# Performance work log

Hardware: AMD Instinct MI355X
Metric: run time of the kernel (lower is better)

Reference implementation:

```python
import jax, jax.numpy as jnp
import numpy as np

SEQ, EMBED, H, QLR, KVLR, RD, VD = 4096, 2048, 16, 512, 512, 64, 128
KD = VD + RD  # full key/query head dim (content + rope)


def _make_rotary_pe(seq_len, dim):
    inv_freq = 1.0 / jnp.power(10000.0, jnp.arange(0, dim, 2) / dim)
    t = jnp.arange(seq_len)
    freqs = jnp.outer(t, inv_freq)  # (seq, dim//2)
    return jnp.sin(freqs), jnp.cos(freqs)


def _apply_rope(x, sin, cos):
    # x: (seq, ..., dim); sin/cos: (seq, dim//2)
    d = x.shape[-1] // 2
    x1, x2 = x[..., :d], x[..., d:]
    sin2 = jnp.concatenate([sin, sin], axis=-1)
    cos2 = jnp.concatenate([cos, cos], axis=-1)
    ne = x.ndim - 2
    sin2 = sin2.reshape(sin2.shape[0], *[1] * ne, sin2.shape[1])
    cos2 = cos2.reshape(cos2.shape[0], *[1] * ne, cos2.shape[1])
    rot = jnp.concatenate([-x2, x1], axis=-1)
    return x * cos2 + rot * sin2


def setup_inputs() -> dict:
    key = jax.random.key(0)
    ks = jax.random.split(key, 8)

    def w(k, out_dim, in_dim):
        return jax.random.normal(k, (out_dim, in_dim), dtype=jnp.float32) * (1.0 / np.sqrt(in_dim))

    x = jax.random.normal(ks[0], (SEQ, EMBED), dtype=jnp.float32)
    mask = jnp.tril(jnp.ones((SEQ, SEQ), dtype=bool))  # causal
    return {
        "x": x,
        "mask": mask,
        "w_q_down": w(ks[1], QLR, EMBED),
        "w_q_up": w(ks[2], H * VD, QLR),
        "w_q_rope": w(ks[3], H * RD, QLR),
        "w_kv_down": w(ks[4], KVLR, EMBED),
        "w_kv_up": w(ks[5], H * 2 * VD, KVLR),
        "w_k_rope": w(ks[6], RD, EMBED),
        "w_out": w(ks[7], EMBED, H * VD),
    }


def reference(x, mask, w_q_down, w_q_up, w_q_rope, w_kv_down, w_kv_up, w_k_rope, w_out):
    seq = x.shape[0]
    # query path through low-rank bottleneck
    c_q = x @ w_q_down.T                                   # (S, QLR)
    q_content = (c_q @ w_q_up.T).reshape(seq, H, VD)       # (S, H, VD)
    q_rope = (c_q @ w_q_rope.T).reshape(seq, H, RD)        # (S, H, RD)
    # kv path through shared low-rank bottleneck
    c_kv = x @ w_kv_down.T                                 # (S, KVLR)
    kv = c_kv @ w_kv_up.T                                  # (S, H*2*VD)
    k_content_flat, v_flat = jnp.split(kv, 2, axis=-1)
    k_content = k_content_flat.reshape(seq, H, VD)
    v = v_flat.reshape(seq, H, VD)
    # shared rope key (one per token, broadcast to heads)
    k_rope_shared = (x @ w_k_rope.T)[:, None, :]           # (S, 1, RD)
    sin, cos = _make_rotary_pe(seq, RD)
    q_rope_rot = _apply_rope(q_rope, sin, cos)             # (S, H, RD)
    k_rope_rot = jnp.tile(_apply_rope(k_rope_shared, sin, cos), (1, H, 1))
    q_final = jnp.concatenate([q_content, q_rope_rot], axis=-1)  # (S, H, KD)
    k_final = jnp.concatenate([k_content, k_rope_rot], axis=-1)  # (S, H, KD)
    # values zero-padded to key dim
    v_padded = jnp.concatenate(
        [v, jnp.zeros((seq, H, RD), dtype=v.dtype)], axis=-1)    # (S, H, KD)
    # scaled dot-product attention per head
    scale = 1.0 / jnp.sqrt(jnp.asarray(KD, dtype=x.dtype))
    scores = jnp.einsum("shd,thd->hst", q_final, k_final) * scale  # (H, S, S)
    scores = jnp.where(mask[None, :, :], scores, jnp.asarray(-1e9, dtype=scores.dtype))
    probs = jax.nn.softmax(scores, axis=-1)
    attn = jnp.einsum("hst,thd->shd", probs, v_padded)             # (S, H, KD)
    attn = attn[..., :VD].reshape(seq, H * VD)                     # drop zero-pad dims
    return attn @ w_out.T                                          # (S, EMBED)
```

## Files before the change

### kernel.cpp

```cpp
#include <hip/hip_runtime.h>


#define SEQ   4096
#define EMBED 2048
#define NHEAD 16
#define QLR   512
#define KVLR  512
#define RD    64
#define VD    128
#define KDIM  192

typedef __attribute__((ext_vector_type(8)))  _Float16 half8;
typedef __attribute__((ext_vector_type(4)))  _Float16 half4;
typedef __attribute__((ext_vector_type(4)))  float    f32x4;
typedef __attribute__((ext_vector_type(16))) float    f32x16;
typedef __attribute__((ext_vector_type(2)))  unsigned int uint2v;
typedef __attribute__((ext_vector_type(4)))  unsigned int uint4v;

__device__ __forceinline__ void gload16(void* lds, const void* g) {
    __builtin_amdgcn_global_load_lds(
        (const __attribute__((address_space(1))) void*)g,
        (__attribute__((address_space(3))) void*)lds, 16, 0, 0);
}

__device__ __forceinline__ unsigned int pkh(float a, float b) {
    auto h = __builtin_amdgcn_cvt_pkrtz(a, b);
    return __builtin_bit_cast(unsigned int, h);
}

__global__ __launch_bounds__(256) void cvt_plain(const float* __restrict__ s,
                                                 _Float16* __restrict__ d, int n8) {
    const int i = blockIdx.x * 256 + threadIdx.x;
    if (i >= n8) return;
    const float4 a = reinterpret_cast<const float4*>(s)[i * 2];
    const float4 b = reinterpret_cast<const float4*>(s)[i * 2 + 1];
    half8 r;
    r[0] = (_Float16)a.x; r[1] = (_Float16)a.y; r[2] = (_Float16)a.z; r[3] = (_Float16)a.w;
    r[4] = (_Float16)b.x; r[5] = (_Float16)b.y; r[6] = (_Float16)b.z; r[7] = (_Float16)b.w;
    reinterpret_cast<half8*>(d)[i] = r;
}

__global__ __launch_bounds__(256) void cvt_down(const float* __restrict__ wqd,
                                                const float* __restrict__ wkvd,
                                                const float* __restrict__ wkr,
                                                _Float16* __restrict__ dst) {
    const int i = blockIdx.x * 256 + threadIdx.x;
    if (i >= 1152 * 2048 / 8) return;
    const int e = i * 8, row = e >> 11, col = e & 2047;
    const float* src = row < 512  ? wqd  + (size_t)row * 2048 + col
                     : row < 1024 ? wkvd + (size_t)(row - 512) * 2048 + col
                     : row < 1088 ? wkr  + (size_t)(row - 1024) * 2048 + col
                                  : nullptr;
    half8 r = {};
    if (src) {
        const float4 a = reinterpret_cast<const float4*>(src)[0];
        const float4 b = reinterpret_cast<const float4*>(src)[1];
        r[0] = (_Float16)a.x; r[1] = (_Float16)a.y; r[2] = (_Float16)a.z; r[3] = (_Float16)a.w;
        r[4] = (_Float16)b.x; r[5] = (_Float16)b.y; r[6] = (_Float16)b.z; r[7] = (_Float16)b.w;
    }
    reinterpret_cast<half8*>(dst)[i] = r;
}

__global__ __launch_bounds__(256) void cvt_qup(const float* __restrict__ wqu,
                                               const float* __restrict__ wqr,
                                               _Float16* __restrict__ dst) {
    const int i = blockIdx.x * 256 + threadIdx.x;
    if (i >= 3072 * 512 / 8) return;
    const int e = i * 8, row = e >> 9, col = e & 511;
    const float* src = row < 2048 ? wqu + (size_t)row * 512 + col
                                  : wqr + (size_t)(row - 2048) * 512 + col;
    const float4 a = reinterpret_cast<const float4*>(src)[0];
    const float4 b = reinterpret_cast<const float4*>(src)[1];
    half8 r;
    r[0] = (_Float16)a.x; r[1] = (_Float16)a.y; r[2] = (_Float16)a.z; r[3] = (_Float16)a.w;
    r[4] = (_Float16)b.x; r[5] = (_Float16)b.y; r[6] = (_Float16)b.z; r[7] = (_Float16)b.w;
    reinterpret_cast<half8*>(dst)[i] = r;
}

template <int EPI>
__global__ __launch_bounds__(256) void gemm_f16(const _Float16* __restrict__ A,
                                                const _Float16* __restrict__ B,
                                                _Float16* __restrict__ o0,
                                                _Float16* __restrict__ o1,
                                                _Float16* __restrict__ o2,
                                                float* __restrict__ of,
                                                int M, int N, int K)
{
    __shared__ _Float16 sA[128 * 64];
    __shared__ _Float16 sB[128 * 64];

    const int tid  = threadIdx.x;
    const int wid  = tid >> 6;
    const int lane = tid & 63;
    const int lr   = lane & 15;
    const int lg   = lane >> 4;
    const int row0 = blockIdx.y * 128;
    const int col0 = blockIdx.x * 128;
    const int war  = (wid >> 1) * 64;
    const int wac  = (wid & 1) * 64;

    const int sr = lane >> 3;
    const int sk = (lane & 7) * 8;
    const _Float16* Ab = A + (size_t)(row0 + wid * 8 + sr) * K + sk;
    const _Float16* Bb = B + (size_t)(col0 + wid * 8 + sr) * K + sk;

    f32x4 acc[4][4] = {};

    for (int k0 = 0; k0 < K; k0 += 64) {
#pragma unroll
        for (int i = 0; i < 4; ++i) {
            const int c = i * 4 + wid;
            gload16((char*)sA + c * 1024, Ab + (size_t)i * 32 * K + k0);
            gload16((char*)sB + c * 1024, Bb + (size_t)i * 32 * K + k0);
        }
        __syncthreads();

#pragma unroll
        for (int kk = 0; kk < 64; kk += 32) {
            half8 a[4], b[4];
#pragma unroll
            for (int i = 0; i < 4; ++i)
                a[i] = *reinterpret_cast<const half8*>(&sA[(war + i * 16 + lr) * 64 + kk + lg * 8]);
#pragma unroll
            for (int j = 0; j < 4; ++j)
                b[j] = *reinterpret_cast<const half8*>(&sB[(wac + j * 16 + lr) * 64 + kk + lg * 8]);
            __builtin_amdgcn_s_setprio(1);
#pragma unroll
            for (int i = 0; i < 4; ++i)
#pragma unroll
                for (int j = 0; j < 4; ++j)
                    acc[i][j] = __builtin_amdgcn_mfma_f32_16x16x32_f16(a[i], b[j], acc[i][j], 0, 0, 0);
            __builtin_amdgcn_s_setprio(0);
        }
        __syncthreads();
    }

#pragma unroll
    for (int i = 0; i < 4; ++i)
#pragma unroll
        for (int j = 0; j < 4; ++j) {
            const int grow0 = row0 + war + i * 16 + lg * 4;
            const int gcol  = col0 + wac + j * 16 + lr;
            if constexpr (EPI == 2) {
                if (gcol >= 2048) {
                    half4 pv;
#pragma unroll
                    for (int r = 0; r < 4; ++r) pv[r] = (_Float16)acc[i][j][r];
                    *reinterpret_cast<half4*>(&o1[(size_t)(gcol - 2048) * SEQ + grow0]) = pv;
                    continue;
                }
            }
#pragma unroll
            for (int r = 0; r < 4; ++r) {
                const int grow = grow0 + r;
                const float v = acc[i][j][r];
                if constexpr (EPI == 0) {
                    if (gcol < 512)       o0[(size_t)grow * 512 + gcol] = (_Float16)v;
                    else if (gcol < 1024) o1[(size_t)grow * 512 + gcol - 512] = (_Float16)v;
                    else if (gcol < 1088) o2[(size_t)grow * 64 + gcol - 1024] = (_Float16)v;
                } else if constexpr (EPI == 1) {
                    if (gcol < 2048)
                        o0[(size_t)grow * (NHEAD * KDIM) + (gcol >> 7) * KDIM + (gcol & 127)] = (_Float16)v;
                    else {
                        const int c = gcol - 2048;
                        o0[(size_t)grow * (NHEAD * KDIM) + (c >> 6) * KDIM + VD + (c & 63)] = (_Float16)v;
                    }
                } else if constexpr (EPI == 2) {
                    o0[((size_t)(gcol >> 7) * SEQ + grow) * KDIM + (gcol & 127)] = (_Float16)v;
                } else {
                    of[(size_t)grow * N + gcol] = v;
                }
            }
        }
}

__global__ __launch_bounds__(256) void rope_kernel(_Float16* __restrict__ qf,
                                                   _Float16* __restrict__ kf,
                                                   const _Float16* __restrict__ ktmp)
{
    __shared__ float s_sin[32], s_cos[32];
    const int s   = blockIdx.x;
    const int tid = threadIdx.x;
    if (tid < 32) {
        const double inv = exp(-(double)tid * (log(10000.0) / 32.0));
        const double ang = (double)s * inv;
        s_sin[tid] = (float)sin(ang);
        s_cos[tid] = (float)cos(ang);
    }
    __syncthreads();

    for (int p = tid; p < NHEAD * 32; p += 256) {
        const int h = p >> 5, i = p & 31;
        const size_t base = (size_t)s * (NHEAD * KDIM) + h * KDIM + VD;
        const float x1 = (float)qf[base + i];
        const float x2 = (float)qf[base + 32 + i];
        const float cs = s_cos[i], sn = s_sin[i];
        qf[base + i]      = (_Float16)(x1 * cs - x2 * sn);
        qf[base + 32 + i] = (_Float16)(x2 * cs + x1 * sn);
    }
    if (tid < 32) {
        const int i = tid;
        const float x1 = (float)ktmp[(size_t)s * RD + i];
        const float x2 = (float)ktmp[(size_t)s * RD + 32 + i];
        const float cs = s_cos[i], sn = s_sin[i];
        const _Float16 r1 = (_Float16)(x1 * cs - x2 * sn);
        const _Float16 r2 = (_Float16)(x2 * cs + x1 * sn);
#pragma unroll
        for (int h = 0; h < NHEAD; ++h) {
            const size_t base = ((size_t)h * SEQ + s) * KDIM + VD;
            kf[base + i]      = r1;
            kf[base + 32 + i] = r2;
        }
    }
}

__global__ __launch_bounds__(256, 2) void fattn(const _Float16* __restrict__ qf,
                                                const _Float16* __restrict__ kf,
                                                const _Float16* __restrict__ vT,
                                                _Float16* __restrict__ attn)
{
    __shared__ _Float16 sK[2][64 * 192];
    __shared__ _Float16 sV[128 * 64];

    const int idx = blockIdx.x;
    const int h   = idx & 15;
    const int j   = idx >> 4;
    const int qt  = (j < 16) ? (31 - 2 * j) : (2 * (j - 16));
    const int q0  = qt * 128;

    const int tid  = threadIdx.x;
    const int wid  = tid >> 6;
    const int lane = tid & 63;
    const int l31  = lane & 31;
    const int h5   = lane >> 5;
    const int x7   = l31 & 7;
    const int qg   = q0 + wid * 32 + l31;
    const int q0w  = q0 + wid * 32;

    const float scale = 0.0721687836487032f;

    const _Float16* ksrc[6];
    int klds[6];
#pragma unroll
    for (int i = 0; i < 6; ++i) {
        const int c   = wid * 6 + i;
        const int gi  = c * 64 + lane;
        const int row = gi / 24;
        const int g   = gi % 24;
        ksrc[i] = kf + ((size_t)h * SEQ + row) * KDIM + ((g ^ (row & 7)) << 3);
        klds[i] = c * 1024;
    }
    const _Float16* vsrc[4];
    int vlds[4];
#pragma unroll
    for (int i = 0; i < 4; ++i) {
        const int c = wid * 4 + i;
        const int d = c * 8 + (lane >> 3);
        vsrc[i] = vT + ((size_t)h * VD + d) * SEQ + (((lane & 7) ^ (lane >> 3)) << 3);
        vlds[i] = c * 1024;
    }

    half8 qfr[12];
    {
        const _Float16* qb_ = qf + (size_t)qg * (NHEAD * KDIM) + h * KDIM + h5 * 8;
#pragma unroll
        for (int ks = 0; ks < 12; ++ks)
            qfr[ks] = *reinterpret_cast<const half8*>(qb_ + ks * 16);
    }

    f32x16 o0 = {}, o1 = {}, o2 = {}, o3 = {};
    float m_ = -1e30f, l_ = 0.0f;

    const int nt = 2 * qt + 2;

    {
#pragma unroll
        for (int i = 0; i < 6; ++i) gload16((char*)sK[0] + klds[i], ksrc[i]);
#pragma unroll
        for (int i = 0; i < 4; ++i) gload16((char*)sV + vlds[i], vsrc[i]);
    }
    __syncthreads();

    int cur = 0;
    for (int t = 0; t < nt; ++t) {
        const int j0 = t * 64;

        if (t + 1 < nt) {
            const size_t joff = (size_t)(j0 + 64) * KDIM;
#pragma unroll
            for (int i = 0; i < 6; ++i)
                gload16((char*)sK[cur ^ 1] + klds[i], ksrc[i] + joff);
        }

        f32x16 s0 = {}, s1 = {};
        {
            const char* kb = (const char*)sK[cur];
            __builtin_amdgcn_s_setprio(1);
#pragma unroll
            for (int ks = 0; ks < 12; ++ks) {
                const int go = ((ks * 2 + h5) ^ x7) << 4;
                const half8 ka = *reinterpret_cast<const half8*>(kb + l31 * 384 + go);
                const half8 kc = *reinterpret_cast<const half8*>(kb + (32 + l31) * 384 + go);
                s0 = __builtin_amdgcn_mfma_f32_32x32x16_f16(ka, qfr[ks], s0, 0, 0, 0);
                s1 = __builtin_amdgcn_mfma_f32_32x32x16_f16(kc, qfr[ks], s1, 0, 0, 0);
            }
            __builtin_amdgcn_s_setprio(0);
        }

#pragma unroll
        for (int m = 0; m < 16; ++m) { s0[m] *= scale; s1[m] *= scale; }
        if (j0 + 63 > q0w) {
#pragma unroll
            for (int m = 0; m < 16; ++m) {
                const int kv = j0 + (m & 3) + 8 * (m >> 2) + 4 * h5;
                if (kv > qg)      s0[m] = -3.0e38f;
                if (kv + 32 > qg) s1[m] = -3.0e38f;
            }
        }

        float mx = s0[0];
#pragma unroll
        for (int m = 1; m < 16; ++m) mx = fmaxf(mx, s0[m]);
#pragma unroll
        for (int m = 0; m < 16; ++m) mx = fmaxf(mx, s1[m]);
        mx = fmaxf(mx, __shfl_xor(mx, 32, 64));

        if (!__all(mx - m_ <= 8.0f)) {
            const float mn = fmaxf(m_, mx);
            const float alpha = __expf(m_ - mn);
            m_ = mn;
            l_ *= alpha;
#pragma unroll
            for (int m = 0; m < 16; ++m) {
                o0[m] *= alpha; o1[m] *= alpha; o2[m] *= alpha; o3[m] *= alpha;
            }
        }
        float rs = 0.0f;
#pragma unroll
        for (int m = 0; m < 16; ++m) { const float p = __expf(s0[m] - m_); s0[m] = p; rs += p; }
#pragma unroll
        for (int m = 0; m < 16; ++m) { const float p = __expf(s1[m] - m_); s1[m] = p; rs += p; }
        rs += __shfl_xor(rs, 32, 64);
        l_ += rs;

        half8 pb0, pb1, pb2, pb3;
        {
            unsigned int x, x2, y, y2;
            x  = pkh(s0[0], s0[1]);  x2 = pkh(s0[2], s0[3]);
            y  = pkh(s0[4], s0[5]);  y2 = pkh(s0[6], s0[7]);
            uint2v r1 = __builtin_amdgcn_permlane32_swap(x, y, false, false);
            uint2v r2 = __builtin_amdgcn_permlane32_swap(x2, y2, false, false);
            { uint4v u = { r1[0], r2[0], r1[1], r2[1] }; pb0 = __builtin_bit_cast(half8, u); }
            x  = pkh(s0[8], s0[9]);  x2 = pkh(s0[10], s0[11]);
            y  = pkh(s0[12], s0[13]); y2 = pkh(s0[14], s0[15]);
            r1 = __builtin_amdgcn_permlane32_swap(x, y, false, false);
            r2 = __builtin_amdgcn_permlane32_swap(x2, y2, false, false);
            { uint4v u = { r1[0], r2[0], r1[1], r2[1] }; pb1 = __builtin_bit_cast(half8, u); }
            x  = pkh(s1[0], s1[1]);  x2 = pkh(s1[2], s1[3]);
            y  = pkh(s1[4], s1[5]);  y2 = pkh(s1[6], s1[7]);
            r1 = __builtin_amdgcn_permlane32_swap(x, y, false, false);
            r2 = __builtin_amdgcn_permlane32_swap(x2, y2, false, false);
            { uint4v u = { r1[0], r2[0], r1[1], r2[1] }; pb2 = __builtin_bit_cast(half8, u); }
            x  = pkh(s1[8], s1[9]);  x2 = pkh(s1[10], s1[11]);
            y  = pkh(s1[12], s1[13]); y2 = pkh(s1[14], s1[15]);
            r1 = __builtin_amdgcn_permlane32_swap(x, y, false, false);
            r2 = __builtin_amdgcn_permlane32_swap(x2, y2, false, false);
            { uint4v u = { r1[0], r2[0], r1[1], r2[1] }; pb3 = __builtin_bit_cast(half8, u); }
        }

        __syncthreads();

        {
            const char* vbse = (const char*)sV;
            __builtin_amdgcn_s_setprio(1);
#pragma unroll
            for (int ks = 0; ks < 4; ++ks) {
                const int go = ((ks * 2 + h5) ^ x7) << 4;
                const half8 pbk = ks == 0 ? pb0 : ks == 1 ? pb1 : ks == 2 ? pb2 : pb3;
                const half8 v0 = *reinterpret_cast<const half8*>(vbse + (l31)      * 128 + go);
                const half8 v1 = *reinterpret_cast<const half8*>(vbse + (32 + l31) * 128 + go);
                const half8 v2 = *reinterpret_cast<const half8*>(vbse + (64 + l31) * 128 + go);
                const half8 v3 = *reinterpret_cast<const half8*>(vbse + (96 + l31) * 128 + go);
                o0 = __builtin_amdgcn_mfma_f32_32x32x16_f16(v0, pbk, o0, 0, 0, 0);
                o1 = __builtin_amdgcn_mfma_f32_32x32x16_f16(v1, pbk, o1, 0, 0, 0);
                o2 = __builtin_amdgcn_mfma_f32_32x32x16_f16(v2, pbk, o2, 0, 0, 0);
                o3 = __builtin_amdgcn_mfma_f32_32x32x16_f16(v3, pbk, o3, 0, 0, 0);
            }
            __builtin_amdgcn_s_setprio(0);
        }

        __syncthreads();

        if (t + 1 < nt) {
            const int jn = j0 + 64;
#pragma unroll
            for (int i = 0; i < 4; ++i)
                gload16((char*)sV + vlds[i], vsrc[i] + jn);
        }
        cur ^= 1;
    }

    const float invl = 1.0f / l_;
    _Float16* ob = attn + (size_t)qg * (NHEAD * VD) + h * VD + 4 * h5;
#pragma unroll
    for (int g = 0; g < 4; ++g) {
#pragma unroll
        for (int pp = 0; pp < 2; ++pp) {
            const int m = g * 4 + pp * 2;
            const int dof = pp * 2 + 8 * g;
            *reinterpret_cast<unsigned int*>(ob + dof) =
                pkh(o0[m] * invl, o0[m + 1] * invl);
            *reinterpret_cast<unsigned int*>(ob + 32 + dof) =
                pkh(o1[m] * invl, o1[m + 1] * invl);
            *reinterpret_cast<unsigned int*>(ob + 64 + dof) =
                pkh(o2[m] * invl, o2[m + 1] * invl);
            *reinterpret_cast<unsigned int*>(ob + 96 + dof) =
                pkh(o3[m] * invl, o3[m + 1] * invl);
        }
    }
}

extern "C" void kernel_launch(void* const* d_in, const int* in_sizes, int n_in,
                              void* d_out, int out_size, void* d_ws, size_t ws_size,
                              hipStream_t stream)
{
    (void)in_sizes; (void)n_in; (void)out_size; (void)ws_size;
    const float* x    = (const float*)d_in[0];
    const float* wqd  = (const float*)d_in[2];
    const float* wqu  = (const float*)d_in[3];
    const float* wqr  = (const float*)d_in[4];
    const float* wkvd = (const float*)d_in[5];
    const float* wkvu = (const float*)d_in[6];
    const float* wkr  = (const float*)d_in[7];
    const float* wout = (const float*)d_in[8];
    float* out = (float*)d_out;

    char* ws = (char*)d_ws;
    _Float16* x_h    = (_Float16*)ws; ws += (size_t)SEQ * EMBED * 2;
    _Float16* wdownh = (_Float16*)ws; ws += (size_t)1152 * EMBED * 2;
    _Float16* wquph  = (_Float16*)ws; ws += (size_t)3072 * QLR * 2;
    _Float16* wkvuh  = (_Float16*)ws; ws += (size_t)4096 * KVLR * 2;
    _Float16* c_q    = (_Float16*)ws; ws += (size_t)SEQ * QLR * 2;
    _Float16* c_kv   = (_Float16*)ws; ws += (size_t)SEQ * KVLR * 2;
    _Float16* ktmp   = (_Float16*)ws; ws += (size_t)SEQ * RD * 2;
    _Float16* qfin   = (_Float16*)ws; ws += (size_t)SEQ * NHEAD * KDIM * 2;
    _Float16* kfin   = (_Float16*)ws; ws += (size_t)SEQ * NHEAD * KDIM * 2;
    _Float16* vT     = (_Float16*)ws; ws += (size_t)NHEAD * VD * SEQ * 2;
    _Float16* attn   = x_h;
    _Float16* wouth  = c_q;

    dim3 blk(256);

    cvt_plain<<<dim3(4096), blk, 0, stream>>>(x, x_h, SEQ * EMBED / 8);
    cvt_down <<<dim3(1152), blk, 0, stream>>>(wqd, wkvd, wkr, wdownh);
    cvt_qup  <<<dim3(768),  blk, 0, stream>>>(wqu, wqr, wquph);
    cvt_plain<<<dim3(1024), blk, 0, stream>>>(wkvu, wkvuh, 4096 * KVLR / 8);

    gemm_f16<0><<<dim3(9, 32), blk, 0, stream>>>(
        x_h, wdownh, c_q, c_kv, ktmp, nullptr, SEQ, 1152, EMBED);
    gemm_f16<1><<<dim3(24, 32), blk, 0, stream>>>(
        c_q, wquph, qfin, nullptr, nullptr, nullptr, SEQ, 3072, QLR);
    gemm_f16<2><<<dim3(32, 32), blk, 0, stream>>>(
        c_kv, wkvuh, kfin, vT, nullptr, nullptr, SEQ, 4096, KVLR);

    cvt_plain<<<dim3(2048), blk, 0, stream>>>(wout, wouth, EMBED * EMBED / 8);

    rope_kernel<<<dim3(SEQ), blk, 0, stream>>>(qfin, kfin, ktmp);
    fattn<<<dim3(512), blk, 0, stream>>>(qfin, kfin, vT, attn);
    gemm_f16<3><<<dim3(16, 32), blk, 0, stream>>>(
        attn, wouth, nullptr, nullptr, nullptr, out, SEQ, EMBED, NHEAD * VD);
}
```

Baseline: 335.7 us.

## Fuse conversions, fold RoPE into GEMM epilogues, shrink attention tiles

Merges the four weight/input fp16 conversion launches into one kernel. Removes the separate RoPE kernel by applying rotary embedding in the down-projection and q-up GEMM epilogues, writing the shared rotated key directly into all heads. Restructures flash attention to 128-thread blocks with 64-query tiles and 32-key steps, doubling the grid, to improve load balance and occupancy. Smaller KV steps mean more barriers and loop iterations per tile, and the epilogues now call powf and sincosf per element.

```diff
diff --git a/kernel.cpp b/kernel.cpp
--- a/kernel.cpp
+++ b/kernel.cpp
@@ -28,53 +28,58 @@
     return __builtin_bit_cast(unsigned int, h);
 }
 
+__device__ __forceinline__ half8 cvt8(const float* p) {
+    const float4 a = *reinterpret_cast<const float4*>(p);
+    const float4 b = *reinterpret_cast<const float4*>(p + 4);
+    half8 r;
+    r[0] = (_Float16)a.x; r[1] = (_Float16)a.y; r[2] = (_Float16)a.z; r[3] = (_Float16)a.w;
+    r[4] = (_Float16)b.x; r[5] = (_Float16)b.y; r[6] = (_Float16)b.z; r[7] = (_Float16)b.w;
+    return r;
+}
+
+__global__ __launch_bounds__(256) void cvt_all(const float* __restrict__ x,
+                                               const float* __restrict__ wqd,
+                                               const float* __restrict__ wkvd,
+                                               const float* __restrict__ wkr,
+                                               const float* __restrict__ wqu,
+                                               const float* __restrict__ wqr,
+                                               const float* __restrict__ wkvu,
+                                               _Float16* __restrict__ x_h,
+                                               _Float16* __restrict__ wdownh,
+                                               _Float16* __restrict__ wquph,
+                                               _Float16* __restrict__ wkvuh)
+{
+    const int b = blockIdx.x;
+    if (b < 4096) {
+        const int i = b * 256 + threadIdx.x;
+        reinterpret_cast<half8*>(x_h)[i] = cvt8(x + i * 8);
+    } else if (b < 5248) {
+        const int i = (b - 4096) * 256 + threadIdx.x;
+        const int e = i * 8, row = e >> 11, col = e & 2047;
+        const float* src = row < 512  ? wqd  + (size_t)row * 2048 + col
+                         : row < 1024 ? wkvd + (size_t)(row - 512) * 2048 + col
+                         : row < 1088 ? wkr  + (size_t)(row - 1024) * 2048 + col
+                                      : nullptr;
+        half8 r = {};
+        if (src) r = cvt8(src);
+        reinterpret_cast<half8*>(wdownh)[i] = r;
+    } else if (b < 6016) {
+        const int i = (b - 5248) * 256 + threadIdx.x;
+        const int e = i * 8, row = e >> 9, col = e & 511;
+        const float* src = row < 2048 ? wqu + (size_t)row * 512 + col
+                                      : wqr + (size_t)(row - 2048) * 512 + col;
+        reinterpret_cast<half8*>(wquph)[i] = cvt8(src);
+    } else {
+        const int i = (b - 6016) * 256 + threadIdx.x;
+        reinterpret_cast<half8*>(wkvuh)[i] = cvt8(wkvu + i * 8);
+    }
+}
+
 __global__ __launch_bounds__(256) void cvt_plain(const float* __restrict__ s,
                                                  _Float16* __restrict__ d, int n8) {
     const int i = blockIdx.x * 256 + threadIdx.x;
     if (i >= n8) return;
-    const float4 a = reinterpret_cast<const float4*>(s)[i * 2];
-    const float4 b = reinterpret_cast<const float4*>(s)[i * 2 + 1];
-    half8 r;
-    r[0] = (_Float16)a.x; r[1] = (_Float16)a.y; r[2] = (_Float16)a.z; r[3] = (_Float16)a.w;
-    r[4] = (_Float16)b.x; r[5] = (_Float16)b.y; r[6] = (_Float16)b.z; r[7] = (_Float16)b.w;
-    reinterpret_cast<half8*>(d)[i] = r;
-}
-
-__global__ __launch_bounds__(256) void cvt_down(const float* __restrict__ wqd,
-                                                const float* __restrict__ wkvd,
-                                                const float* __restrict__ wkr,
-                                                _Float16* __restrict__ dst) {
-    const int i = blockIdx.x * 256 + threadIdx.x;
-    if (i >= 1152 * 2048 / 8) return;
-    const int e = i * 8, row = e >> 11, col = e & 2047;
-    const float* src = row < 512  ? wqd  + (size_t)row * 2048 + col
-                     : row < 1024 ? wkvd + (size_t)(row - 512) * 2048 + col
-                     : row < 1088 ? wkr  + (size_t)(row - 1024) * 2048 + col
-                                  : nullptr;
-    half8 r = {};
-    if (src) {
-        const float4 a = reinterpret_cast<const float4*>(src)[0];
-        const float4 b = reinterpret_cast<const float4*>(src)[1];
-        r[0] = (_Float16)a.x; r[1] = (_Float16)a.y; r[2] = (_Float16)a.z; r[3] = (_Float16)a.w;
-        r[4] = (_Float16)b.x; r[5] = (_Float16)b.y; r[6] = (_Float16)b.z; r[7] = (_Float16)b.w;
-    }
-    reinterpret_cast<half8*>(dst)[i] = r;
-}
-
-__global__ __launch_bounds__(256) void cvt_qup(const float* __restrict__ wqu,
-                                               const float* __restrict__ wqr,
-                                               _Float16* __restrict__ dst) {
-    const int i = blockIdx.x * 256 + threadIdx.x;
-    if (i >= 3072 * 512 / 8) return;
-    const int e = i * 8, row = e >> 9, col = e & 511;
-    const float* src = row < 2048 ? wqu + (size_t)row * 512 + col
-                                  : wqr + (size_t)(row - 2048) * 512 + col;
-    const float4 a = reinterpret_cast<const float4*>(src)[0];
-    const float4 b = reinterpret_cast<const float4*>(src)[1];
-    half8 r;
-    r[0] = (_Float16)a.x; r[1] = (_Float16)a.y; r[2] = (_Float16)a.z; r[3] = (_Float16)a.w;
-    r[4] = (_Float16)b.x; r[5] = (_Float16)b.y; r[6] = (_Float16)b.z; r[7] = (_Float16)b.w;
-    reinterpret_cast<half8*>(dst)[i] = r;
+    reinterpret_cast<half8*>(d)[i] = cvt8(s + i * 8);
 }
 
 template <int EPI>
@@ -150,92 +155,93 @@
                     continue;
                 }
             }
+            if constexpr (EPI == 0) {
+                if (gcol >= 1024) {
+                    if (gcol < 1056 && j < 2) {
+                        const int dd = gcol - 1024;
+                        const float invf = powf(10000.0f, -(float)dd * (1.0f / 32.0f));
+#pragma unroll
+                        for (int r = 0; r < 4; ++r) {
+                            const int grow = grow0 + r;
+                            float sn, cs;
+                            sincosf((float)grow * invf, &sn, &cs);
+                            const float x1 = acc[i][j][r];
+                            const float x2 = acc[i][j + 2][r];
+                            const _Float16 r1 = (_Float16)(x1 * cs - x2 * sn);
+                            const _Float16 r2 = (_Float16)(x2 * cs + x1 * sn);
+#pragma unroll
+                            for (int h = 0; h < NHEAD; ++h) {
+                                const size_t base = ((size_t)h * SEQ + grow) * KDIM + VD;
+                                o2[base + dd]      = r1;
+                                o2[base + 32 + dd] = r2;
+                            }
+                        }
+                    }
+                    continue;
+                }
+            }
 #pragma unroll
             for (int r = 0; r < 4; ++r) {
                 const int grow = grow0 + r;
                 const float v = acc[i][j][r];
                 if constexpr (EPI == 0) {
-                    if (gcol < 512)       o0[(size_t)grow * 512 + gcol] = (_Float16)v;
-                    else if (gcol < 1024) o1[(size_t)grow * 512 + gcol - 512] = (_Float16)v;
-                    else if (gcol < 1088) o2[(size_t)grow * 64 + gcol - 1024] = (_Float16)v;
+                    if (gcol < 512) o0[(size_t)grow * 512 + gcol] = (_Float16)v;
+                    else            o1[(size_t)grow * 512 + gcol - 512] = (_Float16)v;
                 } else if constexpr (EPI == 1) {
                     if (gcol < 2048)
                         o0[(size_t)grow * (NHEAD * KDIM) + (gcol >> 7) * KDIM + (gcol & 127)] = (_Float16)v;
-                    else {
-                        const int c = gcol - 2048;
-                        o0[(size_t)grow * (NHEAD * KDIM) + (c >> 6) * KDIM + VD + (c & 63)] = (_Float16)v;
-                    }
                 } else if constexpr (EPI == 2) {
                     o0[((size_t)(gcol >> 7) * SEQ + grow) * KDIM + (gcol & 127)] = (_Float16)v;
                 } else {
                     of[(size_t)grow * N + gcol] = v;
                 }
             }
-        }
-}
-
-__global__ __launch_bounds__(256) void rope_kernel(_Float16* __restrict__ qf,
-                                                   _Float16* __restrict__ kf,
-                                                   const _Float16* __restrict__ ktmp)
-{
-    __shared__ float s_sin[32], s_cos[32];
-    const int s   = blockIdx.x;
-    const int tid = threadIdx.x;
-    if (tid < 32) {
-        const double inv = exp(-(double)tid * (log(10000.0) / 32.0));
-        const double ang = (double)s * inv;
-        s_sin[tid] = (float)sin(ang);
-        s_cos[tid] = (float)cos(ang);
-    }
-    __syncthreads();
-
-    for (int p = tid; p < NHEAD * 32; p += 256) {
-        const int h = p >> 5, i = p & 31;
-        const size_t base = (size_t)s * (NHEAD * KDIM) + h * KDIM + VD;
-        const float x1 = (float)qf[base + i];
-        const float x2 = (float)qf[base + 32 + i];
-        const float cs = s_cos[i], sn = s_sin[i];
-        qf[base + i]      = (_Float16)(x1 * cs - x2 * sn);
-        qf[base + 32 + i] = (_Float16)(x2 * cs + x1 * sn);
-    }
-    if (tid < 32) {
-        const int i = tid;
-        const float x1 = (float)ktmp[(size_t)s * RD + i];
-        const float x2 = (float)ktmp[(size_t)s * RD + 32 + i];
-        const float cs = s_cos[i], sn = s_sin[i];
-        const _Float16 r1 = (_Float16)(x1 * cs - x2 * sn);
-        const _Float16 r2 = (_Float16)(x2 * cs + x1 * sn);
-#pragma unroll
-        for (int h = 0; h < NHEAD; ++h) {
-            const size_t base = ((size_t)h * SEQ + s) * KDIM + VD;
-            kf[base + i]      = r1;
-            kf[base + 32 + i] = r2;
-        }
-    }
-}
-
-__global__ __launch_bounds__(256, 2) void fattn(const _Float16* __restrict__ qf,
+            if constexpr (EPI == 1) {
+                if (gcol >= 2048 && j < 2) {
+                    const int c  = gcol - 2048;
+                    const int hh = c >> 6;
+                    const int dd = c & 63;
+                    const float invf = powf(10000.0f, -(float)dd * (1.0f / 32.0f));
+#pragma unroll
+                    for (int r = 0; r < 4; ++r) {
+                        const int grow = grow0 + r;
+                        float sn, cs;
+                        sincosf((float)grow * invf, &sn, &cs);
+                        const float x1 = acc[i][j][r];
+                        const float x2 = acc[i][j + 2][r];
+                        const size_t base = (size_t)grow * (NHEAD * KDIM) + hh * KDIM + VD;
+                        o0[base + dd]      = (_Float16)(x1 * cs - x2 * sn);
+                        o0[base + 32 + dd] = (_Float16)(x2 * cs + x1 * sn);
+                    }
+                }
+            }
+        }
+}
+
+__global__ __launch_bounds__(128, 2) void fattn(const _Float16* __restrict__ qf,
                                                 const _Float16* __restrict__ kf,
                                                 const _Float16* __restrict__ vT,
                                                 _Float16* __restrict__ attn)
 {
-    __shared__ _Float16 sK[2][64 * 192];
-    __shared__ _Float16 sV[128 * 64];
+    __shared__ _Float16 sK[2][32 * 192];
+    __shared__ _Float16 sV[128 * 32];
 
     const int idx = blockIdx.x;
     const int h   = idx & 15;
     const int j   = idx >> 4;
-    const int qt  = (j < 16) ? (31 - 2 * j) : (2 * (j - 16));
-    const int q0  = qt * 128;
+    const int jb  = j >> 4;
+    const int ja  = j & 15;
+    const int qt  = (jb == 0) ? (63 - ja) : (jb == 1) ? ja
+                  : (jb == 2) ? (47 - ja) : (16 + ja);
+    const int q0  = qt * 64;
 
     const int tid  = threadIdx.x;
     const int wid  = tid >> 6;
     const int lane = tid & 63;
     const int l31  = lane & 31;
     const int h5   = lane >> 5;
-    const int x7   = l31 & 7;
-    const int qg   = q0 + wid * 32 + l31;
     const int q0w  = q0 + wid * 32;
+    const int qg   = q0w + l31;
 
     const float scale = 0.0721687836487032f;
 
@@ -255,8 +261,9 @@
 #pragma unroll
     for (int i = 0; i < 4; ++i) {
         const int c = wid * 4 + i;
-        const int d = c * 8 + (lane >> 3);
-        vsrc[i] = vT + ((size_t)h * VD + d) * SEQ + (((lane & 7) ^ (lane >> 3)) << 3);
+        const int d = c * 16 + (lane >> 2);
+        vsrc[i] = vT + ((size_t)h * VD + d) * SEQ
+                     + (((lane & 3) ^ ((lane >> 3) & 3)) << 3);
         vlds[i] = c * 1024;
     }
 
@@ -273,56 +280,49 @@
 
     const int nt = 2 * qt + 2;
 
-    {
-#pragma unroll
-        for (int i = 0; i < 6; ++i) gload16((char*)sK[0] + klds[i], ksrc[i]);
-#pragma unroll
-        for (int i = 0; i < 4; ++i) gload16((char*)sV + vlds[i], vsrc[i]);
-    }
+#pragma unroll
+    for (int i = 0; i < 6; ++i) gload16((char*)sK[0] + klds[i], ksrc[i]);
+#pragma unroll
+    for (int i = 0; i < 4; ++i) gload16((char*)sV + vlds[i], vsrc[i]);
     __syncthreads();
 
     int cur = 0;
     for (int t = 0; t < nt; ++t) {
-        const int j0 = t * 64;
+        const int j0 = t * 32;
 
         if (t + 1 < nt) {
-            const size_t joff = (size_t)(j0 + 64) * KDIM;
+            const size_t joff = (size_t)(j0 + 32) * KDIM;
 #pragma unroll
             for (int i = 0; i < 6; ++i)
                 gload16((char*)sK[cur ^ 1] + klds[i], ksrc[i] + joff);
         }
 
-        f32x16 s0 = {}, s1 = {};
+        f32x16 s0 = {};
         {
             const char* kb = (const char*)sK[cur];
             __builtin_amdgcn_s_setprio(1);
 #pragma unroll
             for (int ks = 0; ks < 12; ++ks) {
-                const int go = ((ks * 2 + h5) ^ x7) << 4;
+                const int go = (((ks * 2 + h5) ^ (l31 & 7)) << 4);
                 const half8 ka = *reinterpret_cast<const half8*>(kb + l31 * 384 + go);
-                const half8 kc = *reinterpret_cast<const half8*>(kb + (32 + l31) * 384 + go);
                 s0 = __builtin_amdgcn_mfma_f32_32x32x16_f16(ka, qfr[ks], s0, 0, 0, 0);
-                s1 = __builtin_amdgcn_mfma_f32_32x32x16_f16(kc, qfr[ks], s1, 0, 0, 0);
             }
             __builtin_amdgcn_s_setprio(0);
         }
 
 #pragma unroll
-        for (int m = 0; m < 16; ++m) { s0[m] *= scale; s1[m] *= scale; }
-        if (j0 + 63 > q0w) {
+        for (int m = 0; m < 16; ++m) s0[m] *= scale;
+        if (j0 + 31 > q0w) {
 #pragma unroll
             for (int m = 0; m < 16; ++m) {
                 const int kv = j0 + (m & 3) + 8 * (m >> 2) + 4 * h5;
-                if (kv > qg)      s0[m] = -3.0e38f;
-                if (kv + 32 > qg) s1[m] = -3.0e38f;
+                if (kv > qg) s0[m] = -3.0e38f;
             }
         }
 
         float mx = s0[0];
 #pragma unroll
         for (int m = 1; m < 16; ++m) mx = fmaxf(mx, s0[m]);
-#pragma unroll
-        for (int m = 0; m < 16; ++m) mx = fmaxf(mx, s1[m]);
         mx = fmaxf(mx, __shfl_xor(mx, 32, 64));
 
         if (!__all(mx - m_ <= 8.0f)) {
@@ -338,12 +338,10 @@
         float rs = 0.0f;
 #pragma unroll
         for (int m = 0; m < 16; ++m) { const float p = __expf(s0[m] - m_); s0[m] = p; rs += p; }
-#pragma unroll
-        for (int m = 0; m < 16; ++m) { const float p = __expf(s1[m] - m_); s1[m] = p; rs += p; }
         rs += __shfl_xor(rs, 32, 64);
         l_ += rs;
 
-        half8 pb0, pb1, pb2, pb3;
+        half8 pb0, pb1;
         {
             unsigned int x, x2, y, y2;
             x  = pkh(s0[0], s0[1]);  x2 = pkh(s0[2], s0[3]);
@@ -351,21 +349,11 @@
             uint2v r1 = __builtin_amdgcn_permlane32_swap(x, y, false, false);
             uint2v r2 = __builtin_amdgcn_permlane32_swap(x2, y2, false, false);
             { uint4v u = { r1[0], r2[0], r1[1], r2[1] }; pb0 = __builtin_bit_cast(half8, u); }
-            x  = pkh(s0[8], s0[9]);  x2 = pkh(s0[10], s0[11]);
+            x  = pkh(s0[8], s0[9]);   x2 = pkh(s0[10], s0[11]);
             y  = pkh(s0[12], s0[13]); y2 = pkh(s0[14], s0[15]);
             r1 = __builtin_amdgcn_permlane32_swap(x, y, false, false);
             r2 = __builtin_amdgcn_permlane32_swap(x2, y2, false, false);
             { uint4v u = { r1[0], r2[0], r1[1], r2[1] }; pb1 = __builtin_bit_cast(half8, u); }
-            x  = pkh(s1[0], s1[1]);  x2 = pkh(s1[2], s1[3]);
-            y  = pkh(s1[4], s1[5]);  y2 = pkh(s1[6], s1[7]);
-            r1 = __builtin_amdgcn_permlane32_swap(x, y, false, false);
-            r2 = __builtin_amdgcn_permlane32_swap(x2, y2, false, false);
-            { uint4v u = { r1[0], r2[0], r1[1], r2[1] }; pb2 = __builtin_bit_cast(half8, u); }
-            x  = pkh(s1[8], s1[9]);  x2 = pkh(s1[10], s1[11]);
-            y  = pkh(s1[12], s1[13]); y2 = pkh(s1[14], s1[15]);
-            r1 = __builtin_amdgcn_permlane32_swap(x, y, false, false);
-            r2 = __builtin_amdgcn_permlane32_swap(x2, y2, false, false);
-            { uint4v u = { r1[0], r2[0], r1[1], r2[1] }; pb3 = __builtin_bit_cast(half8, u); }
         }
 
         __syncthreads();
@@ -374,13 +362,13 @@
             const char* vbse = (const char*)sV;
             __builtin_amdgcn_s_setprio(1);
 #pragma unroll
-            for (int ks = 0; ks < 4; ++ks) {
-                const int go = ((ks * 2 + h5) ^ x7) << 4;
-                const half8 pbk = ks == 0 ? pb0 : ks == 1 ? pb1 : ks == 2 ? pb2 : pb3;
-                const half8 v0 = *reinterpret_cast<const half8*>(vbse + (l31)      * 128 + go);
-                const half8 v1 = *reinterpret_cast<const half8*>(vbse + (32 + l31) * 128 + go);
-                const half8 v2 = *reinterpret_cast<const half8*>(vbse + (64 + l31) * 128 + go);
-                const half8 v3 = *reinterpret_cast<const half8*>(vbse + (96 + l31) * 128 + go);
+            for (int ks = 0; ks < 2; ++ks) {
+                const int go = (((ks * 2 + h5) ^ ((l31 >> 1) & 3)) << 4);
+                const half8 pbk = ks == 0 ? pb0 : pb1;
+                const half8 v0 = *reinterpret_cast<const half8*>(vbse + (l31)      * 64 + go);
+                const half8 v1 = *reinterpret_cast<const half8*>(vbse + (32 + l31) * 64 + go);
+                const half8 v2 = *reinterpret_cast<const half8*>(vbse + (64 + l31) * 64 + go);
+                const half8 v3 = *reinterpret_cast<const half8*>(vbse + (96 + l31) * 64 + go);
                 o0 = __builtin_amdgcn_mfma_f32_32x32x16_f16(v0, pbk, o0, 0, 0, 0);
                 o1 = __builtin_amdgcn_mfma_f32_32x32x16_f16(v1, pbk, o1, 0, 0, 0);
                 o2 = __builtin_amdgcn_mfma_f32_32x32x16_f16(v2, pbk, o2, 0, 0, 0);
@@ -392,7 +380,7 @@
         __syncthreads();
 
         if (t + 1 < nt) {
-            const int jn = j0 + 64;
+            const int jn = j0 + 32;
 #pragma unroll
             for (int i = 0; i < 4; ++i)
                 gload16((char*)sV + vlds[i], vsrc[i] + jn);
@@ -442,7 +430,6 @@
     _Float16* wkvuh  = (_Float16*)ws; ws += (size_t)4096 * KVLR * 2;
     _Float16* c_q    = (_Float16*)ws; ws += (size_t)SEQ * QLR * 2;
     _Float16* c_kv   = (_Float16*)ws; ws += (size_t)SEQ * KVLR * 2;
-    _Float16* ktmp   = (_Float16*)ws; ws += (size_t)SEQ * RD * 2;
     _Float16* qfin   = (_Float16*)ws; ws += (size_t)SEQ * NHEAD * KDIM * 2;
     _Float16* kfin   = (_Float16*)ws; ws += (size_t)SEQ * NHEAD * KDIM * 2;
     _Float16* vT     = (_Float16*)ws; ws += (size_t)NHEAD * VD * SEQ * 2;
@@ -451,13 +438,11 @@
 
     dim3 blk(256);
 
-    cvt_plain<<<dim3(4096), blk, 0, stream>>>(x, x_h, SEQ * EMBED / 8);
-    cvt_down <<<dim3(1152), blk, 0, stream>>>(wqd, wkvd, wkr, wdownh);
-    cvt_qup  <<<dim3(768),  blk, 0, stream>>>(wqu, wqr, wquph);
-    cvt_plain<<<dim3(1024), blk, 0, stream>>>(wkvu, wkvuh, 4096 * KVLR / 8);
+    cvt_all<<<dim3(7040), blk, 0, stream>>>(x, wqd, wkvd, wkr, wqu, wqr, wkvu,
+                                            x_h, wdownh, wquph, wkvuh);
 
     gemm_f16<0><<<dim3(9, 32), blk, 0, stream>>>(
-        x_h, wdownh, c_q, c_kv, ktmp, nullptr, SEQ, 1152, EMBED);
+        x_h, wdownh, c_q, c_kv, kfin, nullptr, SEQ, 1152, EMBED);
     gemm_f16<1><<<dim3(24, 32), blk, 0, stream>>>(
         c_q, wquph, qfin, nullptr, nullptr, nullptr, SEQ, 3072, QLR);
     gemm_f16<2><<<dim3(32, 32), blk, 0, stream>>>(
@@ -465,8 +450,7 @@
 
     cvt_plain<<<dim3(2048), blk, 0, stream>>>(wout, wouth, EMBED * EMBED / 8);
 
-    rope_kernel<<<dim3(SEQ), blk, 0, stream>>>(qfin, kfin, ktmp);
-    fattn<<<dim3(512), blk, 0, stream>>>(qfin, kfin, vT, attn);
+    fattn<<<dim3(1024), dim3(128), 0, stream>>>(qfin, kfin, vT, attn);
     gemm_f16<3><<<dim3(16, 32), blk, 0, stream>>>(
         attn, wouth, nullptr, nullptr, nullptr, out, SEQ, EMBED, NHEAD * VD);
 }
```

New measurement: 695.2 us. +107.1%, slower.
